# Kernel tuning notes

Hardware: AMD Instinct MI355X
Metric: run time of the kernel (lower is better)

## Reference

```python
import jax, jax.numpy as jnp
import numpy as np

MAX_TIMESTEPS = 100
EPS_VAR = 1e-8
EPS_DEN = 1e-8

def setup_inputs() -> dict:
    key = jax.random.key(0)
    k1, k2, k3, k4, k5 = jax.random.split(key, 5)
    b, c, h, w = 64, 3, 256, 256
    data = jax.random.normal(k1, (b, c, h, w), dtype=jnp.float32)
    noise = jax.random.normal(k2, (b, c, h, w), dtype=jnp.float32)
    times = jax.random.uniform(k3, (b,), dtype=jnp.float32)
    pred_mean = jax.random.normal(k4, (b, c, h, w), dtype=jnp.float32)
    pred_log_var = jax.random.normal(k5, (b, c, h, w), dtype=jnp.float32)
    return {"data": data, "noise": noise, "times": times,
            "pred_mean": pred_mean, "pred_log_var": pred_log_var}

def reference(data, noise, times, pred_mean, pred_log_var):
    b = data.shape[0]
    # times scaled as in forward: t * (1 - max_timesteps^-1)
    t = times * (1.0 - MAX_TIMESTEPS ** (-1))          # [b]
    t4 = t[:, None, None, None]                         # [b,1,1,1]
    tb = t[:, None]                                     # [b,1]

    # noised = noise.lerp(data, t) = noise + t*(data - noise)
    noised = noise + t4 * (data - noise)                # [b,c,h,w]

    d_flat = data.reshape(b, -1)                        # [j, d]
    n_flat = noised.reshape(b, -1)                      # [b, d]

    # dist[b,j] = sum_chw (noised_b - t_b * data_j)^2 / (2 * var_b)
    # expanded to avoid materializing [b,j,c,h,w]:
    var = (1.0 - tb) ** 2 + EPS_VAR                     # [b,1]
    n2 = jnp.sum(n_flat * n_flat, axis=-1, keepdims=True)   # [b,1]
    d2 = jnp.sum(d_flat * d_flat, axis=-1)                   # [j]
    cross = n_flat @ d_flat.T                                # [b,j]
    dist = (n2 - 2.0 * tb * cross + (tb ** 2) * d2[None, :]) / (2.0 * var)

    weights = jax.nn.softmax(-dist, axis=1)             # [b,j]

    # u_hat = sum_j w_bj (data_j - noised_b) / (1 - t_b + eps)
    #       = (weights @ data - noised) / (1 - t_b + eps)   (weights row-sum to 1)
    mix = weights @ d_flat                              # [b,d]
    u_hat = ((mix - n_flat) / (1.0 - tb + EPS_DEN)).reshape(data.shape)

    flow_cond = data - noise
    correction = jax.lax.stop_gradient(u_hat ** 2 - flow_cond ** 2)

    pred_var = jnp.exp(pred_log_var)
    loss = ((pred_mean - flow_cond) ** 2 / (2.0 * pred_var)
            + 0.5 * pred_log_var
            + correction / (2.0 * pred_var))
    loss = jax.lax.stop_gradient(pred_var) * loss
    return loss.mean()
```

## Files before the change

kernel.cpp:

```cpp
#include <hip/hip_runtime.h>
#include <cstdint>

namespace {

constexpr int BB = 64;
constexpr int DDIM = 196608;
constexpr float T_SCALE = 0.99f;

constexpr int WS_ZD   = 0;
constexpr int WS_DD   = 4096;
constexpr int WS_Z2   = 8192;
constexpr int WS_ELEM = 8256;
constexpr int NRED    = 8257;
constexpr int WS_U2   = 8320;
constexpr int WS_BIGP = 8384;
constexpr int PSTRIDE = 8272;

using f32x4  = __attribute__((ext_vector_type(4))) float;
using bf16x8 = __attribute__((ext_vector_type(8))) __bf16;

__device__ inline f32x4 MFMA(bf16x8 a, bf16x8 b, f32x4 c) {
  return __builtin_amdgcn_mfma_f32_16x16x32_bf16(a, b, c, 0, 0, 0);
}

__global__ void k_init(float* __restrict__ ws) {
  int idx = blockIdx.x * 256 + threadIdx.x;
  if (idx < NRED) ws[idx] = 0.0f;
}

template <int SUBT, bool ATOMIC>
__global__ __launch_bounds__(256) void k_main(
    const float* __restrict__ data, const float* __restrict__ noise,
    const float* __restrict__ pmean, const float* __restrict__ plogv,
    float* __restrict__ ws, float* __restrict__ bigp) {
  __shared__ __align__(16) short lds[6 * 4096];
  __shared__ float esm[4];

  const int t  = threadIdx.x;
  const int wv = t >> 6;
  const int l  = t & 63;
  const int m0 = wv << 4;
  const int sr = t >> 2;
  const int kq = (t & 3) << 4;
  const int chunk0 = blockIdx.x * (SUBT << 6);
  float* dst = ATOMIC ? ws : (bigp + (size_t)blockIdx.x * PSTRIDE);

  f32x4 zdacc[4], ddacc[4];
#pragma unroll
  for (int b = 0; b < 4; ++b) { zdacc[b] = 0.0f; ddacc[b] = 0.0f; }
  float z2acc = 0.0f, eacc = 0.0f;
  float4 dv[4], zv[4];

  auto LOAD = [&](int s) {
    const size_t base = (size_t)sr * DDIM + chunk0 + (s << 6) + kq;
#pragma unroll
    for (int i = 0; i < 4; ++i) {
      dv[i] = *(const float4*)(data  + base + (i << 2));
      zv[i] = *(const float4*)(noise + base + (i << 2));
    }
  };

  auto SPLIT = [&](const float4* v, int tbase) {
    uint32_t hi[8], mi[8], lo[8];
#pragma unroll
    for (int p = 0; p < 8; ++p) {
      const float a = ((const float*)v)[2 * p];
      const float b = ((const float*)v)[2 * p + 1];
      const uint32_t ha = __float_as_uint(a) & 0xFFFF0000u;
      const uint32_t hb = __float_as_uint(b) & 0xFFFF0000u;
      hi[p] = (ha >> 16) | hb;
      const float ra = a - __uint_as_float(ha);
      const float rb = b - __uint_as_float(hb);
      const uint32_t ma = __float_as_uint(ra) & 0xFFFF0000u;
      const uint32_t mb = __float_as_uint(rb) & 0xFFFF0000u;
      mi[p] = (ma >> 16) | mb;
      const float sa = ra - __uint_as_float(ma);
      const float sb = rb - __uint_as_float(mb);
      lo[p] = (__float_as_uint(sa) >> 16) |
              (__float_as_uint(sb) & 0xFFFF0000u);
    }
    const int c0 = kq >> 3;
    const int sw = sr & 7;
    char* base = (char*)lds;
#pragma unroll
    for (int sp = 0; sp < 3; ++sp) {
      const uint32_t* pk = (sp == 0) ? hi : (sp == 1) ? mi : lo;
      uint4 w0 = {pk[0], pk[1], pk[2], pk[3]};
      uint4 w1 = {pk[4], pk[5], pk[6], pk[7]};
      *(uint4*)(base + (tbase + sp) * 8192 + sr * 128 + ((c0 ^ sw) << 4)) = w0;
      *(uint4*)(base + (tbase + sp) * 8192 + sr * 128 +
                (((c0 + 1) ^ sw) << 4)) = w1;
    }
  };

  auto WRITE = [&](int s) {
    const size_t base = (size_t)sr * DDIM + chunk0 + (s << 6) + kq;
    float4 pmv[4], plv[4];
#pragma unroll
    for (int i = 0; i < 4; ++i) {
      pmv[i] = *(const float4*)(pmean + base + (i << 2));
      plv[i] = *(const float4*)(plogv + base + (i << 2));
    }
    SPLIT(zv, 0);
    SPLIT(dv, 3);
#pragma unroll
    for (int p = 0; p < 16; ++p) {
      const float d  = ((const float*)dv)[p];
      const float z  = ((const float*)zv)[p];
      const float pm = ((const float*)pmv)[p];
      const float pl = ((const float*)plv)[p];
      const float fc = d - z;
      eacc += 0.5f * (pm * pm + __expf(pl) * pl) - pm * fc;
      z2acc += z * z;
    }
  };

  LOAD(0);
  WRITE(0);
  for (int s = 0; s < SUBT; ++s) {
    if (s + 1 < SUBT) LOAD(s + 1);
    __syncthreads();
#pragma unroll
    for (int s2 = 0; s2 < 2; ++s2) {
      const int rA   = m0 + (l & 15);
      const int cA   = (s2 << 2) + (l >> 4);
      const int offA = rA * 128 + ((cA ^ (rA & 7)) << 4);
      bf16x8 az[3], ad[3];
#pragma unroll
      for (int sp = 0; sp < 3; ++sp) {
        az[sp] = *(const bf16x8*)((const char*)lds + sp * 8192 + offA);
        ad[sp] = *(const bf16x8*)((const char*)lds + (3 + sp) * 8192 + offA);
      }
#pragma unroll
      for (int b = 0; b < 4; ++b) {
        const int rB   = (b << 4) + (l & 15);
        const int offB = rB * 128 + ((cA ^ (rB & 7)) << 4);
        bf16x8 bd[3];
#pragma unroll
        for (int sp = 0; sp < 3; ++sp)
          bd[sp] = *(const bf16x8*)((const char*)lds + (3 + sp) * 8192 + offB);
        zdacc[b] = MFMA(az[0], bd[0], zdacc[b]);
        zdacc[b] = MFMA(az[0], bd[1], zdacc[b]);
        zdacc[b] = MFMA(az[1], bd[0], zdacc[b]);
        zdacc[b] = MFMA(az[1], bd[1], zdacc[b]);
        zdacc[b] = MFMA(az[0], bd[2], zdacc[b]);
        zdacc[b] = MFMA(az[2], bd[0], zdacc[b]);
        ddacc[b] = MFMA(ad[0], bd[0], ddacc[b]);
        ddacc[b] = MFMA(ad[0], bd[1], ddacc[b]);
        ddacc[b] = MFMA(ad[1], bd[0], ddacc[b]);
        ddacc[b] = MFMA(ad[1], bd[1], ddacc[b]);
        ddacc[b] = MFMA(ad[0], bd[2], ddacc[b]);
        ddacc[b] = MFMA(ad[2], bd[0], ddacc[b]);
      }
    }
    __syncthreads();
    if (s + 1 < SUBT) WRITE(s + 1);
  }

  {
    float v = z2acc;
    v += __shfl_xor(v, 1);
    v += __shfl_xor(v, 2);
    if ((l & 3) == 0) {
      if (ATOMIC) atomicAdd(ws + WS_Z2 + sr, v);
      else        dst[WS_Z2 + sr] = v;
    }
  }
  {
    float ev = eacc;
#pragma unroll
    for (int m = 1; m <= 32; m <<= 1) ev += __shfl_xor(ev, m);
    if (l == 0) esm[wv] = ev;
  }
  __syncthreads();
  if (t == 0) {
    const float s0 = esm[0] + esm[1] + esm[2] + esm[3];
    if (ATOMIC) atomicAdd(ws + WS_ELEM, s0);
    else        dst[WS_ELEM] = s0;
  }

#pragma unroll
  for (int b = 0; b < 4; ++b)
#pragma unroll
    for (int rg = 0; rg < 4; ++rg) {
      const int row = m0 + ((l >> 4) << 2) + rg;
      const int col = (b << 4) + (l & 15);
      if (ATOMIC) {
        atomicAdd(ws + WS_ZD + row * 64 + col, zdacc[b][rg]);
        atomicAdd(ws + WS_DD + row * 64 + col, ddacc[b][rg]);
      } else {
        dst[WS_ZD + row * 64 + col] = zdacc[b][rg];
        dst[WS_DD + row * 64 + col] = ddacc[b][rg];
      }
    }
}

__global__ void k_reduce(const float* __restrict__ bigp, float* __restrict__ ws,
                         int nb) {
  const int idx = blockIdx.x * 64 + threadIdx.x;
  if (idx >= NRED) return;
  const int per = nb >> 3;
  const size_t b0 = (size_t)blockIdx.y * per;
  float s = 0.f;
#pragma unroll 4
  for (int b = 0; b < per; ++b)
    s += bigp[(b0 + b) * PSTRIDE + idx];
  atomicAdd(ws + idx, s);
}

__global__ void k_small(const float* __restrict__ times, float* __restrict__ ws) {
  const int i = blockIdx.x;
  const int j = threadIdx.x;
  const double tt = (double)(times[i] * T_SCALE);
  const double omt = 1.0 - tt;
  const double var = omt * omt + 1e-8;
  const double inv2v = 1.0 / (2.0 * var);
  const double zd = (double)ws[WS_ZD + (i << 6) + j];
  const double dd = (double)ws[WS_DD + (i << 6) + j];
  const double cross = omt * zd + tt * dd;
  const double d2j = (double)ws[WS_DD + j * 65];
  const double lg = (2.0 * tt * cross - tt * tt * d2j) * inv2v;
  double m = lg;
#pragma unroll
  for (int msk = 1; msk <= 32; msk <<= 1) m = fmax(m, __shfl_xor(m, msk));
  const double e = exp(lg - m);
  double S = e;
#pragma unroll
  for (int msk = 1; msk <= 32; msk <<= 1) S += __shfl_xor(S, msk);
  const double wgt = e / S;

  __shared__ double wsh[64];
  wsh[j] = wgt;
  __syncthreads();
  double inner = 0.0;
#pragma unroll 8
  for (int j2 = 0; j2 < 64; ++j2)
    inner += wsh[j2] * (double)ws[WS_DD + (j << 6) + j2];
  double s1 = wgt * inner;
  double s2 = wgt * cross;
#pragma unroll
  for (int msk = 1; msk <= 32; msk <<= 1) {
    s1 += __shfl_xor(s1, msk);
    s2 += __shfl_xor(s2, msk);
  }
  if (j == 0) {
    const double zdii = (double)ws[WS_ZD + i * 65];
    const double d2i  = (double)ws[WS_DD + i * 65];
    const double z2i  = (double)ws[WS_Z2 + i];
    const double n2   = omt * omt * z2i + 2.0 * tt * omt * zdii + tt * tt * d2i;
    const double den  = omt + 1e-8;
    ws[WS_U2 + i] = (float)((s1 - 2.0 * s2 + n2) / (den * den));
  }
}

__global__ void k_final(const float* __restrict__ ws, float* __restrict__ out) {
  const int t = threadIdx.x;
  double v = 0.5 * (double)ws[WS_U2 + t];
  if (t == 0) v += (double)ws[WS_ELEM];
#pragma unroll
  for (int m = 1; m <= 32; m <<= 1) v += __shfl_xor(v, m);
  if (t == 0) out[0] = (float)(v / (double)((size_t)BB * DDIM));
}

}

extern "C" void kernel_launch(void* const* d_in, const int* in_sizes, int n_in,
                              void* d_out, int out_size, void* d_ws, size_t ws_size,
                              hipStream_t stream) {
  const float* data  = (const float*)d_in[0];
  const float* noise = (const float*)d_in[1];
  const float* times = (const float*)d_in[2];
  const float* pmean = (const float*)d_in[3];
  const float* plogv = (const float*)d_in[4];
  float* out = (float*)d_out;
  float* ws  = (float*)d_ws;
  float* bigp = ws + WS_BIGP;

  auto fits = [&](long long nb) {
    return ws_size >= ((size_t)WS_BIGP + (size_t)nb * PSTRIDE) * sizeof(float);
  };

  k_init<<<dim3(33), dim3(256), 0, stream>>>(ws);
  if (fits(1024)) {
    k_main<3, false><<<dim3(1024), dim3(256), 0, stream>>>(
        data, noise, pmean, plogv, ws, bigp);
    k_reduce<<<dim3(130, 8), dim3(64), 0, stream>>>(bigp, ws, 1024);
  } else if (fits(512)) {
    k_main<6, false><<<dim3(512), dim3(256), 0, stream>>>(
        data, noise, pmean, plogv, ws, bigp);
    k_reduce<<<dim3(130, 8), dim3(64), 0, stream>>>(bigp, ws, 512);
  } else {
    k_main<6, true><<<dim3(512), dim3(256), 0, stream>>>(
        data, noise, pmean, plogv, ws, bigp);
  }
  k_small<<<dim3(64), dim3(64), 0, stream>>>(times, ws);
  k_final<<<dim3(1), dim3(64), 0, stream>>>(ws, out);
}
```

Baseline: 67.32 us.

## Split Gram accumulation across two wave groups with 512-thread blocks and deeper prefetch

Doubles block size to 512 threads, with the first four waves accumulating the noise-data Gram block and the other four the data-data block. Each wave now runs half as many MFMAs, and each thread loads and splits half as many elements. The loop is reordered so the bf16 split of the next tile runs during the MMA phase, and global loads for the tile after that are issued early. The 1024-block path is dropped, so the kernel now always uses 512 blocks with 6 sub-tiles. This adds an extra barrier per iteration and more registers held across the MMA phase.

```diff
diff --git a/kernel.cpp b/kernel.cpp
--- a/kernel.cpp
+++ b/kernel.cpp
@@ -29,108 +29,99 @@
 }
 
 template <int SUBT, bool ATOMIC>
-__global__ __launch_bounds__(256) void k_main(
+__global__ __launch_bounds__(512) void k_main(
     const float* __restrict__ data, const float* __restrict__ noise,
     const float* __restrict__ pmean, const float* __restrict__ plogv,
     float* __restrict__ ws, float* __restrict__ bigp) {
   __shared__ __align__(16) short lds[6 * 4096];
-  __shared__ float esm[4];
+  __shared__ float esm[8];
 
   const int t  = threadIdx.x;
   const int wv = t >> 6;
   const int l  = t & 63;
-  const int m0 = wv << 4;
-  const int sr = t >> 2;
-  const int kq = (t & 3) << 4;
+  const int g  = wv >> 2;
+  const int m0 = (wv & 3) << 4;
+  const int sr = t >> 3;
+  const int c0 = t & 7;
   const int chunk0 = blockIdx.x * (SUBT << 6);
   float* dst = ATOMIC ? ws : (bigp + (size_t)blockIdx.x * PSTRIDE);
 
-  f32x4 zdacc[4], ddacc[4];
-#pragma unroll
-  for (int b = 0; b < 4; ++b) { zdacc[b] = 0.0f; ddacc[b] = 0.0f; }
+  f32x4 acc[4];
+#pragma unroll
+  for (int b = 0; b < 4; ++b) acc[b] = 0.0f;
   float z2acc = 0.0f, eacc = 0.0f;
-  float4 dv[4], zv[4];
+  float4 dv[2], zv[2], pv[2], gv[2];
+  uint4 sZ[3], sD[3];
 
   auto LOAD = [&](int s) {
-    const size_t base = (size_t)sr * DDIM + chunk0 + (s << 6) + kq;
-#pragma unroll
-    for (int i = 0; i < 4; ++i) {
+    const size_t base = (size_t)sr * DDIM + chunk0 + (s << 6) + (c0 << 3);
+#pragma unroll
+    for (int i = 0; i < 2; ++i) {
       dv[i] = *(const float4*)(data  + base + (i << 2));
       zv[i] = *(const float4*)(noise + base + (i << 2));
-    }
-  };
-
-  auto SPLIT = [&](const float4* v, int tbase) {
-    uint32_t hi[8], mi[8], lo[8];
-#pragma unroll
-    for (int p = 0; p < 8; ++p) {
-      const float a = ((const float*)v)[2 * p];
-      const float b = ((const float*)v)[2 * p + 1];
+      pv[i] = *(const float4*)(pmean + base + (i << 2));
+      gv[i] = *(const float4*)(plogv + base + (i << 2));
+    }
+  };
+
+  auto SPLIT8 = [&](const float4* v, uint4& H, uint4& M, uint4& L) {
+    uint32_t h[4], m[4], lo[4];
+    const float* f = (const float*)v;
+#pragma unroll
+    for (int p = 0; p < 4; ++p) {
+      const float a = f[2 * p], b = f[2 * p + 1];
       const uint32_t ha = __float_as_uint(a) & 0xFFFF0000u;
       const uint32_t hb = __float_as_uint(b) & 0xFFFF0000u;
-      hi[p] = (ha >> 16) | hb;
+      h[p] = (ha >> 16) | hb;
       const float ra = a - __uint_as_float(ha);
       const float rb = b - __uint_as_float(hb);
       const uint32_t ma = __float_as_uint(ra) & 0xFFFF0000u;
       const uint32_t mb = __float_as_uint(rb) & 0xFFFF0000u;
-      mi[p] = (ma >> 16) | mb;
+      m[p] = (ma >> 16) | mb;
       const float sa = ra - __uint_as_float(ma);
       const float sb = rb - __uint_as_float(mb);
-      lo[p] = (__float_as_uint(sa) >> 16) |
-              (__float_as_uint(sb) & 0xFFFF0000u);
-    }
-    const int c0 = kq >> 3;
-    const int sw = sr & 7;
-    char* base = (char*)lds;
-#pragma unroll
-    for (int sp = 0; sp < 3; ++sp) {
-      const uint32_t* pk = (sp == 0) ? hi : (sp == 1) ? mi : lo;
-      uint4 w0 = {pk[0], pk[1], pk[2], pk[3]};
-      uint4 w1 = {pk[4], pk[5], pk[6], pk[7]};
-      *(uint4*)(base + (tbase + sp) * 8192 + sr * 128 + ((c0 ^ sw) << 4)) = w0;
-      *(uint4*)(base + (tbase + sp) * 8192 + sr * 128 +
-                (((c0 + 1) ^ sw) << 4)) = w1;
-    }
-  };
-
-  auto WRITE = [&](int s) {
-    const size_t base = (size_t)sr * DDIM + chunk0 + (s << 6) + kq;
-    float4 pmv[4], plv[4];
-#pragma unroll
-    for (int i = 0; i < 4; ++i) {
-      pmv[i] = *(const float4*)(pmean + base + (i << 2));
-      plv[i] = *(const float4*)(plogv + base + (i << 2));
-    }
-    SPLIT(zv, 0);
-    SPLIT(dv, 3);
-#pragma unroll
-    for (int p = 0; p < 16; ++p) {
-      const float d  = ((const float*)dv)[p];
-      const float z  = ((const float*)zv)[p];
-      const float pm = ((const float*)pmv)[p];
-      const float pl = ((const float*)plv)[p];
+      lo[p] = (__float_as_uint(sa) >> 16) | (__float_as_uint(sb) & 0xFFFF0000u);
+    }
+    H = uint4{h[0], h[1], h[2], h[3]};
+    M = uint4{m[0], m[1], m[2], m[3]};
+    L = uint4{lo[0], lo[1], lo[2], lo[3]};
+  };
+
+  auto SPLITCALC = [&]() {
+    const float* df = (const float*)dv;
+    const float* zf = (const float*)zv;
+    const float* pf = (const float*)pv;
+    const float* gf = (const float*)gv;
+#pragma unroll
+    for (int p = 0; p < 8; ++p) {
+      const float d = df[p], z = zf[p], pm = pf[p], pl = gf[p];
       const float fc = d - z;
       eacc += 0.5f * (pm * pm + __expf(pl) * pl) - pm * fc;
       z2acc += z * z;
     }
-  };
-
-  LOAD(0);
-  WRITE(0);
-  for (int s = 0; s < SUBT; ++s) {
-    if (s + 1 < SUBT) LOAD(s + 1);
-    __syncthreads();
+    SPLIT8(zv, sZ[0], sZ[1], sZ[2]);
+    SPLIT8(dv, sD[0], sD[1], sD[2]);
+  };
+
+  auto DSW = [&]() {
+    char* base = (char*)lds + sr * 128 + ((c0 ^ (sr & 7)) << 4);
+#pragma unroll
+    for (int sp = 0; sp < 3; ++sp) {
+      *(uint4*)(base + sp * 8192)       = sZ[sp];
+      *(uint4*)(base + (3 + sp) * 8192) = sD[sp];
+    }
+  };
+
+  auto MMA = [&]() {
 #pragma unroll
     for (int s2 = 0; s2 < 2; ++s2) {
       const int rA   = m0 + (l & 15);
       const int cA   = (s2 << 2) + (l >> 4);
       const int offA = rA * 128 + ((cA ^ (rA & 7)) << 4);
-      bf16x8 az[3], ad[3];
-#pragma unroll
-      for (int sp = 0; sp < 3; ++sp) {
-        az[sp] = *(const bf16x8*)((const char*)lds + sp * 8192 + offA);
-        ad[sp] = *(const bf16x8*)((const char*)lds + (3 + sp) * 8192 + offA);
-      }
+      bf16x8 af[3];
+#pragma unroll
+      for (int sp = 0; sp < 3; ++sp)
+        af[sp] = *(const bf16x8*)((const char*)lds + (g * 3 + sp) * 8192 + offA);
 #pragma unroll
       for (int b = 0; b < 4; ++b) {
         const int rB   = (b << 4) + (l & 15);
@@ -139,29 +130,39 @@
 #pragma unroll
         for (int sp = 0; sp < 3; ++sp)
           bd[sp] = *(const bf16x8*)((const char*)lds + (3 + sp) * 8192 + offB);
-        zdacc[b] = MFMA(az[0], bd[0], zdacc[b]);
-        zdacc[b] = MFMA(az[0], bd[1], zdacc[b]);
-        zdacc[b] = MFMA(az[1], bd[0], zdacc[b]);
-        zdacc[b] = MFMA(az[1], bd[1], zdacc[b]);
-        zdacc[b] = MFMA(az[0], bd[2], zdacc[b]);
-        zdacc[b] = MFMA(az[2], bd[0], zdacc[b]);
-        ddacc[b] = MFMA(ad[0], bd[0], ddacc[b]);
-        ddacc[b] = MFMA(ad[0], bd[1], ddacc[b]);
-        ddacc[b] = MFMA(ad[1], bd[0], ddacc[b]);
-        ddacc[b] = MFMA(ad[1], bd[1], ddacc[b]);
-        ddacc[b] = MFMA(ad[0], bd[2], ddacc[b]);
-        ddacc[b] = MFMA(ad[2], bd[0], ddacc[b]);
+        acc[b] = MFMA(af[0], bd[0], acc[b]);
+        acc[b] = MFMA(af[0], bd[1], acc[b]);
+        acc[b] = MFMA(af[1], bd[0], acc[b]);
+        acc[b] = MFMA(af[1], bd[1], acc[b]);
+        acc[b] = MFMA(af[0], bd[2], acc[b]);
+        acc[b] = MFMA(af[2], bd[0], acc[b]);
       }
     }
+  };
+
+  LOAD(0);
+  SPLITCALC();
+  DSW();
+  LOAD(1);
+  __syncthreads();
+
+  for (int s = 0; s < SUBT; ++s) {
+    if (s + 1 < SUBT) SPLITCALC();
+    MMA();
     __syncthreads();
-    if (s + 1 < SUBT) WRITE(s + 1);
+    if (s + 1 < SUBT) {
+      DSW();
+      if (s + 2 < SUBT) LOAD(s + 2);
+      __syncthreads();
+    }
   }
 
   {
     float v = z2acc;
     v += __shfl_xor(v, 1);
     v += __shfl_xor(v, 2);
-    if ((l & 3) == 0) {
+    v += __shfl_xor(v, 4);
+    if ((l & 7) == 0) {
       if (ATOMIC) atomicAdd(ws + WS_Z2 + sr, v);
       else        dst[WS_Z2 + sr] = v;
     }
@@ -174,24 +175,22 @@
   }
   __syncthreads();
   if (t == 0) {
-    const float s0 = esm[0] + esm[1] + esm[2] + esm[3];
+    float s0 = 0.f;
+#pragma unroll
+    for (int e = 0; e < 8; ++e) s0 += esm[e];
     if (ATOMIC) atomicAdd(ws + WS_ELEM, s0);
     else        dst[WS_ELEM] = s0;
   }
 
+  const int grOff = (g == 0) ? WS_ZD : WS_DD;
 #pragma unroll
   for (int b = 0; b < 4; ++b)
 #pragma unroll
     for (int rg = 0; rg < 4; ++rg) {
       const int row = m0 + ((l >> 4) << 2) + rg;
       const int col = (b << 4) + (l & 15);
-      if (ATOMIC) {
-        atomicAdd(ws + WS_ZD + row * 64 + col, zdacc[b][rg]);
-        atomicAdd(ws + WS_DD + row * 64 + col, ddacc[b][rg]);
-      } else {
-        dst[WS_ZD + row * 64 + col] = zdacc[b][rg];
-        dst[WS_DD + row * 64 + col] = ddacc[b][rg];
-      }
+      if (ATOMIC) atomicAdd(ws + grOff + row * 64 + col, acc[b][rg]);
+      else        dst[grOff + row * 64 + col] = acc[b][rg];
     }
 }
 
@@ -276,21 +275,16 @@
   float* ws  = (float*)d_ws;
   float* bigp = ws + WS_BIGP;
 
-  auto fits = [&](long long nb) {
-    return ws_size >= ((size_t)WS_BIGP + (size_t)nb * PSTRIDE) * sizeof(float);
-  };
+  const bool fits512 =
+      ws_size >= ((size_t)WS_BIGP + (size_t)512 * PSTRIDE) * sizeof(float);
 
   k_init<<<dim3(33), dim3(256), 0, stream>>>(ws);
-  if (fits(1024)) {
-    k_main<3, false><<<dim3(1024), dim3(256), 0, stream>>>(
-        data, noise, pmean, plogv, ws, bigp);
-    k_reduce<<<dim3(130, 8), dim3(64), 0, stream>>>(bigp, ws, 1024);
-  } else if (fits(512)) {
-    k_main<6, false><<<dim3(512), dim3(256), 0, stream>>>(
+  if (fits512) {
+    k_main<6, false><<<dim3(512), dim3(512), 0, stream>>>(
         data, noise, pmean, plogv, ws, bigp);
     k_reduce<<<dim3(130, 8), dim3(64), 0, stream>>>(bigp, ws, 512);
   } else {
-    k_main<6, true><<<dim3(512), dim3(256), 0, stream>>>(
+    k_main<6, true><<<dim3(512), dim3(512), 0, stream>>>(
         data, noise, pmean, plogv, ws, bigp);
   }
   k_small<<<dim3(64), dim3(64), 0, stream>>>(times, ws);
```

New measurement: 58.84 us, median of 3. 12.6% less time.
